# Optimization experiments

Hardware: AMD Instinct MI355X
Metric: run time of the kernel (lower is better)

## Reference

```python
import jax, jax.numpy as jnp
import numpy as np

N = 200000      # number of source simplices (columns of B)
M_SEG = 100000  # number of target simplices (rows of B)
NNZ = 400000    # ~2 nonzeros per column for a boundary operator
C_IN = 256
C_OUT = 256


def setup_inputs() -> dict:
    key = jax.random.key(0)
    k1, k2, k3, k4, k5 = jax.random.split(key, 5)
    x_src = jax.random.normal(k1, (N, C_IN), dtype=jnp.float32)
    W = jax.random.normal(k2, (C_IN, C_OUT), dtype=jnp.float32) / np.sqrt(C_IN)
    b_vals = jax.random.normal(k3, (NNZ,), dtype=jnp.float32)
    b_rows = jax.random.randint(k4, (NNZ,), 0, M_SEG, dtype=jnp.int32)
    b_cols = jax.random.randint(k5, (NNZ,), 0, N, dtype=jnp.int32)
    return {"x_src": x_src, "W": W, "b_vals": b_vals,
            "b_rows": b_rows, "b_cols": b_cols, "M": M_SEG}


def reference(x_src, W, b_vals, b_rows, b_cols, M):
    # Dense projection: nn.Linear(in, out, bias=False) -> x @ W
    x_proj = x_src @ W                                  # [N, C_out]
    # Sparse boundary matmul: out[r] += v * x_proj[c] for each (r, c, v) in B
    msgs = b_vals[:, None] * x_proj[b_cols]             # [nnz, C_out] gather
    out = jax.ops.segment_sum(msgs, b_rows, num_segments=M)  # [M, C_out] scatter-add
    return out
```

## Files before the change

kernel.cpp:

```cpp
#include <hip/hip_runtime.h>


typedef short bf16x8 __attribute__((ext_vector_type(8)));
typedef float f32x4  __attribute__((ext_vector_type(4)));

#define BM 64

static __device__ __forceinline__ unsigned short f2bf(float f) {
    union { float f; unsigned u; } a; a.f = f;
    unsigned r = a.u + 0x7FFFu + ((a.u >> 16) & 1u);
    return (unsigned short)(r >> 16);
}

__global__ __launch_bounds__(256) void wtrans_kernel(
    const float* __restrict__ W, unsigned short* __restrict__ Wt)
{
    int k = blockIdx.x;
    int n = threadIdx.x;
    Wt[(size_t)n * 256 + k] = f2bf(W[(size_t)k * 256 + n]);
}

__global__ __launch_bounds__(256) void hist_kernel(
    const int* __restrict__ b_rows, int* __restrict__ cnt, int nnz)
{
    int i = blockIdx.x * 256 + threadIdx.x;
    if (i < nnz) atomicAdd(&cnt[b_rows[i]], 1);
}

__global__ __launch_bounds__(1024) void scan_part_kernel(
    const int* __restrict__ cnt, int* __restrict__ partials, int M)
{
    int tid = threadIdx.x;
    int base = blockIdx.x * 4096;
    int s = 0;
    #pragma unroll
    for (int k = 0; k < 4; ++k) {
        int i = base + k * 1024 + tid;
        if (i < M) s += cnt[i];
    }
    #pragma unroll
    for (int d = 1; d < 64; d <<= 1) s += __shfl_xor(s, d);
    __shared__ int wsum[16];
    int lane = tid & 63, wid = tid >> 6;
    if (lane == 0) wsum[wid] = s;
    __syncthreads();
    if (tid == 0) {
        int t = 0;
        #pragma unroll
        for (int w = 0; w < 16; ++w) t += wsum[w];
        partials[blockIdx.x] = t;
    }
}

__global__ __launch_bounds__(64) void scan_mid_kernel(
    int* __restrict__ partials, int* __restrict__ off, int np, int M)
{
    int lane = threadIdx.x;
    int v = (lane < np) ? partials[lane] : 0;
    int x = v;
    #pragma unroll
    for (int d = 1; d < 64; d <<= 1) { int y = __shfl_up(x, d); if (lane >= d) x += y; }
    if (lane < np) partials[lane] = x - v;
    if (lane == 63) off[M] = x;
}

__global__ __launch_bounds__(1024) void scan_apply_kernel(
    const int* __restrict__ cnt, const int* __restrict__ partials,
    int* __restrict__ off, int* __restrict__ cursor, int M)
{
    int tid = threadIdx.x;
    int base = blockIdx.x * 4096 + tid * 4;
    int4 v = make_int4(0, 0, 0, 0);
    if (base + 3 < M) v = *reinterpret_cast<const int4*>(cnt + base);
    else {
        if (base + 0 < M) v.x = cnt[base + 0];
        if (base + 1 < M) v.y = cnt[base + 1];
        if (base + 2 < M) v.z = cnt[base + 2];
    }
    int s1 = v.x + v.y, s2 = s1 + v.z, tsum = s2 + v.w;
    int x = tsum;
    int lane = tid & 63, wid = tid >> 6;
    #pragma unroll
    for (int d = 1; d < 64; d <<= 1) { int y = __shfl_up(x, d); if (lane >= d) x += y; }
    __shared__ int wsum[16];
    if (lane == 63) wsum[wid] = x;
    __syncthreads();
    if (wid == 0 && lane < 16) {
        int w = wsum[lane];
        int xx = w;
        #pragma unroll
        for (int d = 1; d < 16; d <<= 1) { int y = __shfl_up(xx, d); if (lane >= d) xx += y; }
        wsum[lane] = xx - w;
    }
    __syncthreads();
    int excl = (x - tsum) + wsum[wid] + partials[blockIdx.x];
    int o0 = excl, o1 = excl + v.x, o2 = excl + s1, o3 = excl + s2;
    if (base + 0 < M) { off[base + 0] = o0; cursor[base + 0] = o0; }
    if (base + 1 < M) { off[base + 1] = o1; cursor[base + 1] = o1; }
    if (base + 2 < M) { off[base + 2] = o2; cursor[base + 2] = o2; }
    if (base + 3 < M) { off[base + 3] = o3; cursor[base + 3] = o3; }
}

__global__ __launch_bounds__(256) void fill_kernel(
    const float* __restrict__ b_vals, const int* __restrict__ b_rows,
    const int* __restrict__ b_cols, int* __restrict__ cursor,
    int* __restrict__ csr_col, float* __restrict__ csr_val, int nnz)
{
    int i = blockIdx.x * 256 + threadIdx.x;
    if (i < nnz) {
        int r = b_rows[i];
        int pos = atomicAdd(&cursor[r], 1);
        csr_col[pos] = b_cols[i];
        csr_val[pos] = b_vals[i];
    }
}

__global__ __launch_bounds__(256) void fused_kernel(
    const float* __restrict__ x_src, const float* __restrict__ csr_val,
    const int* __restrict__ csr_col, const int* __restrict__ off,
    const unsigned short* __restrict__ Wt, float* __restrict__ out, int M)
{
    __shared__ __align__(16) unsigned char Alds[BM * 512];

    int lane = threadIdx.x & 63;
    int wid  = threadIdx.x >> 6;
    int r0   = blockIdx.x * BM;

    const float4* x4 = reinterpret_cast<const float4*>(x_src);
    for (int i = 0; i < 16; ++i) {
        int row = wid * 16 + i;
        int r = r0 + row;
        float4 acc = make_float4(0.f, 0.f, 0.f, 0.f);
        if (r < M) {
            int s = off[r], e = off[r + 1];
            for (int j = s; j < e; ++j) {
                int c = csr_col[j];
                float v = csr_val[j];
                float4 xs = x4[(size_t)c * 64 + lane];
                acc.x += v * xs.x; acc.y += v * xs.y;
                acc.z += v * xs.z; acc.w += v * xs.w;
            }
        }
        ushort4 h;
        h.x = f2bf(acc.x); h.y = f2bf(acc.y); h.z = f2bf(acc.z); h.w = f2bf(acc.w);
        int byte = row * 512 + lane * 8;
        byte ^= (row & 7) << 4;
        *reinterpret_cast<ushort4*>(Alds + byte) = h;
    }
    __syncthreads();

    f32x4 acc[4][4] = {};
    const char* wt = reinterpret_cast<const char*>(Wt);
    int nbase = wid * 64;
    int arow15 = lane & 15;
    int kgrp   = (lane >> 4) * 16;

    for (int s = 0; s < 8; ++s) {
        bf16x8 a[4], b[4];
        #pragma unroll
        for (int m = 0; m < 4; ++m) {
            int row = m * 16 + arow15;
            int byte = row * 512 + s * 64 + kgrp;
            byte ^= (row & 7) << 4;
            a[m] = *reinterpret_cast<const bf16x8*>(Alds + byte);
        }
        #pragma unroll
        for (int t = 0; t < 4; ++t) {
            int n = nbase + t * 16 + arow15;
            b[t] = *reinterpret_cast<const bf16x8*>(wt + (size_t)n * 512 + s * 64 + kgrp);
        }
        #pragma unroll
        for (int m = 0; m < 4; ++m)
            #pragma unroll
            for (int t = 0; t < 4; ++t)
                acc[m][t] = __builtin_amdgcn_mfma_f32_16x16x32_bf16(a[m], b[t], acc[m][t], 0, 0, 0);
    }

    #pragma unroll
    for (int m = 0; m < 4; ++m) {
        int rowb = r0 + m * 16 + (lane >> 4) * 4;
        #pragma unroll
        for (int r = 0; r < 4; ++r) {
            if (rowb + r < M) {
                #pragma unroll
                for (int t = 0; t < 4; ++t)
                    out[(size_t)(rowb + r) * 256 + nbase + t * 16 + arow15] = acc[m][t][r];
            }
        }
    }
}

extern "C" void kernel_launch(void* const* d_in, const int* in_sizes, int n_in,
                              void* d_out, int out_size, void* d_ws, size_t ws_size,
                              hipStream_t stream) {
    const float* x_src  = (const float*)d_in[0];
    const float* W      = (const float*)d_in[1];
    const float* b_vals = (const float*)d_in[2];
    const int*   b_rows = (const int*)d_in[3];
    const int*   b_cols = (const int*)d_in[4];

    const int C = 256;
    const int M = out_size / C;
    const int nnz = in_sizes[2];

    char* ws = (char*)d_ws;
    unsigned short* Wt = (unsigned short*)ws;           ws += 256 * 256 * 2;
    int*   cnt     = (int*)ws;                          ws += (size_t)M * 4;
    int*   off     = (int*)ws;                          ws += (size_t)(M + 1) * 4;
    int*   cursor  = (int*)ws;                          ws += (size_t)M * 4;
    int*   partials= (int*)ws;                          ws += 64 * 4;
    int*   csr_col = (int*)ws;                          ws += (size_t)nnz * 4;
    float* csr_val = (float*)ws;                        ws += (size_t)nnz * 4;

    float* out = (float*)d_out;

    hipMemsetAsync(cnt, 0, (size_t)M * 4, stream);

    wtrans_kernel<<<256, 256, 0, stream>>>(W, Wt);

    int nblk_nnz = (nnz + 255) / 256;
    hist_kernel<<<nblk_nnz, 256, 0, stream>>>(b_rows, cnt, nnz);

    int nb = (M + 4095) / 4096;
    scan_part_kernel<<<nb, 1024, 0, stream>>>(cnt, partials, M);
    scan_mid_kernel<<<1, 64, 0, stream>>>(partials, off, nb, M);
    scan_apply_kernel<<<nb, 1024, 0, stream>>>(cnt, partials, off, cursor, M);

    fill_kernel<<<nblk_nnz, 256, 0, stream>>>(b_vals, b_rows, b_cols, cursor,
                                              csr_col, csr_val, nnz);

    int nblk_fused = (M + BM - 1) / BM;
    fused_kernel<<<nblk_fused, 256, 0, stream>>>(x_src, csr_val, csr_col, off,
                                                 Wt, out, M);
}
```

Before: 236.4 us.

## Make fused gather-GEMM persistent with register-resident W and double-buffered tiles

Replaces the one-block-per-64-rows fused kernel with a persistent grid of 256 blocks of 1024 threads. Each wave holds its 16-column slice of bf16 W in registers for the whole kernel, so W is no longer reloaded from global memory per tile. Each block processes 16-row tiles and prefetches the next tile's sparse gather (up to 8 neighbours batched per step) while running MFMA on the current tile, using a double-buffered LDS tile. The tile count is M/16 with no tail handling, so the kernel assumes M is divisible by 16, and the 1024-thread blocks with many live registers may limit occupancy.

```diff
diff --git a/kernel.cpp b/kernel.cpp
--- a/kernel.cpp
+++ b/kernel.cpp
@@ -4,7 +4,7 @@
 typedef short bf16x8 __attribute__((ext_vector_type(8)));
 typedef float f32x4  __attribute__((ext_vector_type(4)));
 
-#define BM 64
+#define FGRID 256
 
 static __device__ __forceinline__ unsigned short f2bf(float f) {
     union { float f; unsigned u; } a; a.f = f;
@@ -115,78 +115,114 @@
     }
 }
 
-__global__ __launch_bounds__(256) void fused_kernel(
-    const float* __restrict__ x_src, const float* __restrict__ csr_val,
-    const int* __restrict__ csr_col, const int* __restrict__ off,
-    const unsigned short* __restrict__ Wt, float* __restrict__ out, int M)
-{
-    __shared__ __align__(16) unsigned char Alds[BM * 512];
-
-    int lane = threadIdx.x & 63;
-    int wid  = threadIdx.x >> 6;
-    int r0   = blockIdx.x * BM;
-
-    const float4* x4 = reinterpret_cast<const float4*>(x_src);
-    for (int i = 0; i < 16; ++i) {
-        int row = wid * 16 + i;
-        int r = r0 + row;
+#define GATHER_LOAD(row)                                                      \
+    gs = off[row]; ge = off[row + 1];                                         \
+    gn = ge - gs; if (gn > 8) gn = 8;                                         \
+    _Pragma("unroll")                                                         \
+    for (int t = 0; t < 8; ++t)                                               \
+        if (t < gn) { gc[t] = csr_col[gs + t]; gv[t] = csr_val[gs + t]; }     \
+    _Pragma("unroll")                                                         \
+    for (int t = 0; t < 8; ++t)                                               \
+        if (t < gn) gx[t] = x4[(size_t)gc[t] * 64 + lane];
+
+__global__ __launch_bounds__(1024, 4) void fused_kernel(
+    const float* __restrict__ X, const unsigned short* __restrict__ Wt,
+    const float* __restrict__ csr_val, const int* __restrict__ csr_col,
+    const int* __restrict__ off, float* __restrict__ out, int ntiles)
+{
+    __shared__ __align__(16) unsigned char tile[2][16 * 512];
+
+    int tid = threadIdx.x;
+    int lane = tid & 63, w = tid >> 6;
+    int arow = lane & 15, kg = lane >> 4;
+    int xo_w = (w & 7) << 4;
+    int xo_a = (arow & 7) << 4;
+
+    bf16x8 breg[8];
+    {
+        const char* wt = reinterpret_cast<const char*>(Wt);
+        size_t nb = (size_t)(w * 16 + arow) * 512 + kg * 16;
+        #pragma unroll
+        for (int s = 0; s < 8; ++s)
+            breg[s] = *reinterpret_cast<const bf16x8*>(wt + nb + s * 64);
+    }
+
+    const float4* x4 = reinterpret_cast<const float4*>(X);
+
+    int gs, ge, gn;
+    int gc[8]; float gv[8]; float4 gx[8];
+
+    {
+        int row = blockIdx.x * 16 + w;
         float4 acc = make_float4(0.f, 0.f, 0.f, 0.f);
-        if (r < M) {
-            int s = off[r], e = off[r + 1];
-            for (int j = s; j < e; ++j) {
-                int c = csr_col[j];
-                float v = csr_val[j];
-                float4 xs = x4[(size_t)c * 64 + lane];
-                acc.x += v * xs.x; acc.y += v * xs.y;
-                acc.z += v * xs.z; acc.w += v * xs.w;
-            }
+        GATHER_LOAD(row);
+        for (;;) {
+            #pragma unroll
+            for (int t = 0; t < 8; ++t)
+                if (t < gn) {
+                    acc.x += gv[t] * gx[t].x; acc.y += gv[t] * gx[t].y;
+                    acc.z += gv[t] * gx[t].z; acc.w += gv[t] * gx[t].w;
+                }
+            gs += gn;
+            if (gs >= ge) break;
+            gn = ge - gs; if (gn > 8) gn = 8;
+            #pragma unroll
+            for (int t = 0; t < 8; ++t)
+                if (t < gn) { gc[t] = csr_col[gs + t]; gv[t] = csr_val[gs + t]; }
+            #pragma unroll
+            for (int t = 0; t < 8; ++t)
+                if (t < gn) gx[t] = x4[(size_t)gc[t] * 64 + lane];
         }
         ushort4 h;
         h.x = f2bf(acc.x); h.y = f2bf(acc.y); h.z = f2bf(acc.z); h.w = f2bf(acc.w);
-        int byte = row * 512 + lane * 8;
-        byte ^= (row & 7) << 4;
-        *reinterpret_cast<ushort4*>(Alds + byte) = h;
-    }
-    __syncthreads();
-
-    f32x4 acc[4][4] = {};
-    const char* wt = reinterpret_cast<const char*>(Wt);
-    int nbase = wid * 64;
-    int arow15 = lane & 15;
-    int kgrp   = (lane >> 4) * 16;
-
-    for (int s = 0; s < 8; ++s) {
-        bf16x8 a[4], b[4];
-        #pragma unroll
-        for (int m = 0; m < 4; ++m) {
-            int row = m * 16 + arow15;
-            int byte = row * 512 + s * 64 + kgrp;
-            byte ^= (row & 7) << 4;
-            a[m] = *reinterpret_cast<const bf16x8*>(Alds + byte);
+        *reinterpret_cast<ushort4*>(tile[0] + w * 512 + ((lane * 8) ^ xo_w)) = h;
+    }
+    __syncthreads();
+
+    for (int r = 0;; ++r) {
+        int it  = blockIdx.x + r * FGRID;
+        int itn = it + FGRID;
+        bool hasn = (itn < ntiles);
+        int p = r & 1;
+
+        if (hasn) { int row = itn * 16 + w; GATHER_LOAD(row); }
+
+        f32x4 macc = {};
+        #pragma unroll
+        for (int s = 0; s < 8; ++s) {
+            bf16x8 a = *reinterpret_cast<const bf16x8*>(
+                tile[p] + arow * 512 + ((s * 64 + kg * 16) ^ xo_a));
+            macc = __builtin_amdgcn_mfma_f32_16x16x32_bf16(a, breg[s], macc, 0, 0, 0);
         }
-        #pragma unroll
-        for (int t = 0; t < 4; ++t) {
-            int n = nbase + t * 16 + arow15;
-            b[t] = *reinterpret_cast<const bf16x8*>(wt + (size_t)n * 512 + s * 64 + kgrp);
+        int R = it * 16;
+        #pragma unroll
+        for (int rr = 0; rr < 4; ++rr)
+            out[(size_t)(R + kg * 4 + rr) * 256 + w * 16 + arow] = macc[rr];
+
+        if (!hasn) break;
+
+        float4 acc = make_float4(0.f, 0.f, 0.f, 0.f);
+        for (;;) {
+            #pragma unroll
+            for (int t = 0; t < 8; ++t)
+                if (t < gn) {
+                    acc.x += gv[t] * gx[t].x; acc.y += gv[t] * gx[t].y;
+                    acc.z += gv[t] * gx[t].z; acc.w += gv[t] * gx[t].w;
+                }
+            gs += gn;
+            if (gs >= ge) break;
+            gn = ge - gs; if (gn > 8) gn = 8;
+            #pragma unroll
+            for (int t = 0; t < 8; ++t)
+                if (t < gn) { gc[t] = csr_col[gs + t]; gv[t] = csr_val[gs + t]; }
+            #pragma unroll
+            for (int t = 0; t < 8; ++t)
+                if (t < gn) gx[t] = x4[(size_t)gc[t] * 64 + lane];
         }
-        #pragma unroll
-        for (int m = 0; m < 4; ++m)
-            #pragma unroll
-            for (int t = 0; t < 4; ++t)
-                acc[m][t] = __builtin_amdgcn_mfma_f32_16x16x32_bf16(a[m], b[t], acc[m][t], 0, 0, 0);
-    }
-
-    #pragma unroll
-    for (int m = 0; m < 4; ++m) {
-        int rowb = r0 + m * 16 + (lane >> 4) * 4;
-        #pragma unroll
-        for (int r = 0; r < 4; ++r) {
-            if (rowb + r < M) {
-                #pragma unroll
-                for (int t = 0; t < 4; ++t)
-                    out[(size_t)(rowb + r) * 256 + nbase + t * 16 + arow15] = acc[m][t][r];
-            }
-        }
+        ushort4 h;
+        h.x = f2bf(acc.x); h.y = f2bf(acc.y); h.z = f2bf(acc.z); h.w = f2bf(acc.w);
+        *reinterpret_cast<ushort4*>(tile[p ^ 1] + w * 512 + ((lane * 8) ^ xo_w)) = h;
+        __syncthreads();
     }
 }
 
@@ -229,7 +265,7 @@
     fill_kernel<<<nblk_nnz, 256, 0, stream>>>(b_vals, b_rows, b_cols, cursor,
                                               csr_col, csr_val, nnz);
 
-    int nblk_fused = (M + BM - 1) / BM;
-    fused_kernel<<<nblk_fused, 256, 0, stream>>>(x_src, csr_val, csr_col, off,
-                                                 Wt, out, M);
-}
+    int ntiles = M / 16;
+    fused_kernel<<<FGRID, 1024, 0, stream>>>(x_src, Wt, csr_val, csr_col, off,
+                                             out, ntiles);
+}
```

After: 244.8 us. 3.5% more time.
